# Kernel optimization log

Measured on AMD Instinct MI355X. Metric: run time of the kernel, lower is better.

## Reference

```python
import jax, jax.numpy as jnp
import numpy as np

N_NODES = 50000
N_EDGES = 800000
IN_CH = 128
HIDDEN = [128, 128]
OUT_CH = 64


def _glorot(key, shape):
    fan_in, fan_out = shape
    lim = (6.0 / (fan_in + fan_out)) ** 0.5
    return jax.random.uniform(key, shape, jnp.float32, -lim, lim)


def setup_inputs() -> dict:
    key = jax.random.key(0)
    ks = jax.random.split(key, 12)
    x = jax.random.normal(ks[0], (N_NODES, IN_CH), jnp.float32)
    edge_index = jax.random.randint(ks[1], (2, N_EDGES), 0, N_NODES, jnp.int64)
    dims = [IN_CH] + HIDDEN + [OUT_CH]
    params = {}
    for i in range(len(dims) - 1):
        d_in, d_out = dims[i], dims[i + 1]
        params[f"W_l{i}"] = _glorot(ks[2 + 3 * i], (d_in, d_out))      # neighbor weight
        params[f"W_r{i}"] = _glorot(ks[3 + 3 * i], (d_in, d_out))      # root/self weight
        params[f"b{i}"] = jnp.zeros((d_out,), jnp.float32)
    return {"x": x, "edge_index": edge_index, **params}


def _sage_conv(x, src, dst, W_l, W_r, b):
    # mean-aggregate neighbor features: messages flow src -> dst
    n = x.shape[0]
    agg = jax.ops.segment_sum(x[src], dst, num_segments=n)            # [N, d_in]
    cnt = jax.ops.segment_sum(jnp.ones((src.shape[0],), x.dtype), dst, num_segments=n)
    mean = agg / jnp.maximum(cnt, 1.0)[:, None]
    # PyG SAGEConv: lin_l(mean_neighbors) + lin_r(x_self); bias on lin_l only
    return mean @ W_l + x @ W_r + b


def reference(x, edge_index,
              W_l0, W_r0, b0,
              W_l1, W_r1, b1,
              W_l2, W_r2, b2):
    src, dst = edge_index[0], edge_index[1]
    h = _sage_conv(x, src, dst, W_l0, W_r0, b0)
    h = jax.nn.elu(h)
    h = _sage_conv(h, src, dst, W_l1, W_r1, b1)
    h = jax.nn.elu(h)
    out = _sage_conv(h, src, dst, W_l2, W_r2, b2)
    return out
```

## Files before the change

### kernel.cpp

```cpp
#include <hip/hip_runtime.h>
#include <math.h>

#define N_NODES 50000
#define N_EDGES 800000
#define IN_CH 128
#define NBUCK 196
#define BCAP 5120
#define EPB 4082

typedef unsigned short ushort_t;
typedef unsigned int uint_t;
typedef __attribute__((ext_vector_type(8))) short bf16x8;
typedef __attribute__((ext_vector_type(4))) float f32x4;

static __device__ __forceinline__ ushort_t f32_to_bf16(float f) {
    uint_t u = __float_as_uint(f);
    uint_t r = (u + 0x7fffu + ((u >> 16) & 1u)) >> 16;
    return (ushort_t)r;
}
static __device__ __forceinline__ float bf16_to_f32(ushort_t u) {
    return __uint_as_float(((uint_t)u) << 16);
}

static __device__ __forceinline__ bf16x8 cvt8(const float* __restrict__ p) {
    float4 lo = *(const float4*)p;
    float4 hi = *(const float4*)(p + 4);
    bf16x8 r;
    r[0] = (short)f32_to_bf16(lo.x); r[1] = (short)f32_to_bf16(lo.y);
    r[2] = (short)f32_to_bf16(lo.z); r[3] = (short)f32_to_bf16(lo.w);
    r[4] = (short)f32_to_bf16(hi.x); r[5] = (short)f32_to_bf16(hi.y);
    r[6] = (short)f32_to_bf16(hi.z); r[7] = (short)f32_to_bf16(hi.w);
    return r;
}

__global__ __launch_bounds__(256) void binA(
    const int* __restrict__ src, const int* __restrict__ dst,
    uint_t* __restrict__ gbcnt, uint_t* __restrict__ gbuck) {
    __shared__ uint_t hist[NBUCK];
    __shared__ uint_t excl_s[NBUCK];
    __shared__ uint_t gbase[NBUCK];
    __shared__ uint_t cur[NBUCK];
    __shared__ uint_t pfx[256];
    __shared__ uint_t stage[4096];
    __shared__ uint_t gpos[4096];
    const int t = threadIdx.x;
    const int e0 = blockIdx.x * EPB;
    const int e1 = min(e0 + EPB, N_EDGES);

    for (int i = t; i < NBUCK; i += 256) hist[i] = 0;
    __syncthreads();
    for (int e = e0 + t; e < e1; e += 256) atomicAdd(&hist[dst[e] >> 8], 1u);
    __syncthreads();
    uint_t own = (t < NBUCK) ? hist[t] : 0;
    pfx[t] = own;
    __syncthreads();
    for (int d = 1; d < 256; d <<= 1) {
        uint_t v = (t >= d) ? pfx[t - d] : 0;
        __syncthreads();
        pfx[t] += v;
        __syncthreads();
    }
    if (t < NBUCK) {
        uint_t excl = pfx[t] - own;
        excl_s[t] = excl;
        cur[t] = excl;
        gbase[t] = atomicAdd(&gbcnt[t], own);
    }
    __syncthreads();
    for (int e = e0 + t; e < e1; e += 256) {
        int d_ = dst[e];
        int b = d_ >> 8;
        uint_t p = atomicAdd(&cur[b], 1u);
        stage[p] = ((uint_t)(d_ & 255) << 16) | (uint_t)src[e];
        gpos[p] = (uint_t)b * BCAP + gbase[b] + (p - excl_s[b]);
    }
    __syncthreads();
    const int n = e1 - e0;
    for (int i = t; i < n; i += 256) gbuck[gpos[i]] = stage[i];
}

__global__ __launch_bounds__(256) void binB1(
    const uint_t* __restrict__ gbcnt, const uint_t* __restrict__ gbuck,
    int* __restrict__ degi) {
    __shared__ uint_t h[256];
    const int b = blockIdx.x;
    const int t = threadIdx.x;
    h[t] = 0;
    __syncthreads();
    const uint_t n = gbcnt[b];
    const uint_t* p = &gbuck[(size_t)b * BCAP];
    for (uint_t i = t; i < n; i += 256) atomicAdd(&h[(p[i] >> 16) & 255u], 1u);
    __syncthreads();
    int node = b * 256 + t;
    if (node < N_NODES) degi[node] = (int)h[t];
}

__global__ __launch_bounds__(256) void scan_p1(const int* __restrict__ degi,
                                               int* __restrict__ bsum, int n) {
    __shared__ int s[256];
    const int t = threadIdx.x;
    const int i = blockIdx.x * 256 + t;
    s[t] = (i < n) ? degi[i] : 0;
    __syncthreads();
    for (int d = 128; d > 0; d >>= 1) {
        if (t < d) s[t] += s[t + d];
        __syncthreads();
    }
    if (t == 0) bsum[blockIdx.x] = s[0];
}

__global__ __launch_bounds__(256) void scan_p2(int* __restrict__ bsum, int nb) {
    __shared__ int s[256];
    const int t = threadIdx.x;
    int v = (t < nb) ? bsum[t] : 0;
    s[t] = v;
    __syncthreads();
    for (int d = 1; d < 256; d <<= 1) {
        int u = (t >= d) ? s[t - d] : 0;
        __syncthreads();
        s[t] += u;
        __syncthreads();
    }
    if (t < nb) bsum[t] = s[t] - v;
}

__global__ __launch_bounds__(256) void scan_p3(const int* __restrict__ degi,
                                               const int* __restrict__ bsum,
                                               int* __restrict__ offs, int n) {
    __shared__ int s[256];
    const int t = threadIdx.x;
    const int i = blockIdx.x * 256 + t;
    int v = (i < n) ? degi[i] : 0;
    s[t] = v;
    __syncthreads();
    for (int d = 1; d < 256; d <<= 1) {
        int u = (t >= d) ? s[t - d] : 0;
        __syncthreads();
        s[t] += u;
        __syncthreads();
    }
    if (i < n) offs[i] = s[t] - v + bsum[blockIdx.x];
    if (i == 0) offs[n] = N_EDGES;
}

__global__ __launch_bounds__(256) void binB2(
    const uint_t* __restrict__ gbcnt, const uint_t* __restrict__ gbuck,
    const int* __restrict__ offs, int* __restrict__ ebuf) {
    __shared__ int cur[256];
    __shared__ int stage[BCAP];
    const int b = blockIdx.x;
    const int t = threadIdx.x;
    const int node = b * 256 + t;
    const int obase = offs[b * 256];
    cur[t] = (node < N_NODES) ? (offs[node] - obase) : 0;
    __syncthreads();
    const uint_t n = gbcnt[b];
    const uint_t* p = &gbuck[(size_t)b * BCAP];
    for (uint_t i = t; i < n; i += 256) {
        uint_t pr_ = p[i];
        int l = (pr_ >> 16) & 255;
        int pos = atomicAdd(&cur[l], 1);
        stage[pos] = (int)(pr_ & 0xFFFFu);
    }
    __syncthreads();
    for (uint_t i = t; i < n; i += 256) ebuf[obase + (int)i] = stage[i];
}

template <int D_OUT>
__global__ __launch_bounds__(256) void prep_w(const float* __restrict__ Wl,
                                              const float* __restrict__ Wr,
                                              ushort_t* __restrict__ Bt) {
    int i = blockIdx.x * 256 + threadIdx.x;
    if (i >= 2 * D_OUT * IN_CH) return;
    int c = i / IN_CH, k = i % IN_CH;
    float v = (c < D_OUT) ? Wl[(size_t)k * D_OUT + c] : Wr[(size_t)k * D_OUT + (c - D_OUT)];
    Bt[i] = f32_to_bf16(v);
}

template <int D_OUT, bool IN_F32, bool PL_F32>
__global__ __launch_bounds__(256) void gemm_mfma(
    const void* __restrict__ in_v, const ushort_t* __restrict__ Bt,
    const float* __restrict__ bias,
    void* __restrict__ pl_v, float* __restrict__ pr, int nNodes) {
    constexpr int C = 2 * D_OUT;
    constexpr int SLAB = C / 4;
    constexpr int NI = SLAB / 16;
    const int tid = threadIdx.x;
    const int wave = tid >> 6, lane = tid & 63;
    const int node0 = blockIdx.x * 64;
    const int wcol0 = wave * SLAB;
    const int lrow = lane & 15;
    const int lgrp = lane >> 4;

    const ushort_t* inb = (const ushort_t*)in_v;
    const float* inf = (const float*)in_v;

    f32x4 acc[4][NI] = {};

    for (int ks = 0; ks < 4; ++ks) {
        const int k0 = ks * 32 + lgrp * 8;
        bf16x8 a[4];
#pragma unroll
        for (int mi = 0; mi < 4; ++mi) {
            int r = node0 + mi * 16 + lrow;
            r = min(r, nNodes - 1);
            if (IN_F32) {
                a[mi] = cvt8(&inf[(size_t)r * IN_CH + k0]);
            } else {
                a[mi] = *(const bf16x8*)&inb[(size_t)r * IN_CH + k0];
            }
        }
        bf16x8 bf[NI];
#pragma unroll
        for (int ni = 0; ni < NI; ++ni) {
            int c = wcol0 + ni * 16 + lrow;
            bf[ni] = *(const bf16x8*)&Bt[(size_t)c * IN_CH + k0];
        }
#pragma unroll
        for (int mi = 0; mi < 4; ++mi)
#pragma unroll
            for (int ni = 0; ni < NI; ++ni)
                acc[mi][ni] = __builtin_amdgcn_mfma_f32_16x16x32_bf16(
                    a[mi], bf[ni], acc[mi][ni], 0, 0, 0);
    }

    const bool is_pr = (wcol0 >= D_OUT);
#pragma unroll
    for (int ni = 0; ni < NI; ++ni) {
        const int c = wcol0 + ni * 16 + lrow;
        const float bv = is_pr ? bias[c - D_OUT] : 0.f;
#pragma unroll
        for (int mi = 0; mi < 4; ++mi) {
#pragma unroll
            for (int j = 0; j < 4; ++j) {
                int r = node0 + mi * 16 + lgrp * 4 + j;
                if (r >= nNodes) continue;
                float v = acc[mi][ni][j];
                if (is_pr) {
                    pr[(size_t)r * D_OUT + (c - D_OUT)] = v + bv;
                } else if (PL_F32) {
                    ((float*)pl_v)[(size_t)r * D_OUT + c] = v;
                } else {
                    ((ushort_t*)pl_v)[(size_t)r * D_OUT + c] = f32_to_bf16(v);
                }
            }
        }
    }
}

__global__ __launch_bounds__(256) void gather128_bf16_kernel(
    const int* __restrict__ offs, const int* __restrict__ ebuf,
    const ushort_t* __restrict__ pl, const float* __restrict__ pr,
    ushort_t* __restrict__ out, int nNodes) {
    const int wid = (int)((blockIdx.x * 256u + threadIdx.x) >> 6);
    const int lane = threadIdx.x & 63;
    if (wid >= nNodes) return;
    const int o0 = offs[wid], o1 = offs[wid + 1];
    const float inv = 1.0f / fmaxf((float)(o1 - o0), 1.0f);
    const int c = lane * 2;

    float ax0 = 0, ay0 = 0, ax1 = 0, ay1 = 0, ax2 = 0, ay2 = 0, ax3 = 0, ay3 = 0;
    int j = o0;
    for (; j + 4 <= o1; j += 4) {
        int s0 = ebuf[j], s1 = ebuf[j + 1], s2 = ebuf[j + 2], s3 = ebuf[j + 3];
        uint_t v0 = *(const uint_t*)&pl[(size_t)s0 * 128 + c];
        uint_t v1 = *(const uint_t*)&pl[(size_t)s1 * 128 + c];
        uint_t v2 = *(const uint_t*)&pl[(size_t)s2 * 128 + c];
        uint_t v3 = *(const uint_t*)&pl[(size_t)s3 * 128 + c];
        ax0 += __uint_as_float(v0 << 16); ay0 += __uint_as_float(v0 & 0xffff0000u);
        ax1 += __uint_as_float(v1 << 16); ay1 += __uint_as_float(v1 & 0xffff0000u);
        ax2 += __uint_as_float(v2 << 16); ay2 += __uint_as_float(v2 & 0xffff0000u);
        ax3 += __uint_as_float(v3 << 16); ay3 += __uint_as_float(v3 & 0xffff0000u);
    }
    for (; j < o1; ++j) {
        uint_t v0 = *(const uint_t*)&pl[(size_t)ebuf[j] * 128 + c];
        ax0 += __uint_as_float(v0 << 16);
        ay0 += __uint_as_float(v0 & 0xffff0000u);
    }
    float vx = (ax0 + ax1 + ax2 + ax3) * inv + pr[(size_t)wid * 128 + c];
    float vy = (ay0 + ay1 + ay2 + ay3) * inv + pr[(size_t)wid * 128 + c + 1];
    vx = vx > 0.f ? vx : expm1f(vx);
    vy = vy > 0.f ? vy : expm1f(vy);
    uint_t packed = (uint_t)f32_to_bf16(vx) | ((uint_t)f32_to_bf16(vy) << 16);
    *(uint_t*)&out[(size_t)wid * 128 + c] = packed;
}

__global__ __launch_bounds__(256) void gather64_bf16_kernel(
    const int* __restrict__ offs, const int* __restrict__ ebuf,
    const ushort_t* __restrict__ pl, const float* __restrict__ pr,
    float* __restrict__ out, int nNodes) {
    const int wid = (int)((blockIdx.x * 256u + threadIdx.x) >> 6);
    const int lane = threadIdx.x & 63;
    if (wid >= nNodes) return;
    const int o0 = offs[wid], o1 = offs[wid + 1];
    const float inv = 1.0f / fmaxf((float)(o1 - o0), 1.0f);
    const int c = lane;
    float a0 = 0, a1 = 0, a2 = 0, a3 = 0;
    int j = o0;
    for (; j + 4 <= o1; j += 4) {
        int s0 = ebuf[j], s1 = ebuf[j + 1], s2 = ebuf[j + 2], s3 = ebuf[j + 3];
        a0 += bf16_to_f32(pl[(size_t)s0 * 64 + c]);
        a1 += bf16_to_f32(pl[(size_t)s1 * 64 + c]);
        a2 += bf16_to_f32(pl[(size_t)s2 * 64 + c]);
        a3 += bf16_to_f32(pl[(size_t)s3 * 64 + c]);
    }
    for (; j < o1; ++j) a0 += bf16_to_f32(pl[(size_t)ebuf[j] * 64 + c]);
    float v = (a0 + a1 + a2 + a3) * inv + pr[(size_t)wid * 64 + c];
    out[(size_t)wid * 64 + c] = v;
}

extern "C" void kernel_launch(void* const* d_in, const int* in_sizes, int n_in,
                              void* d_out, int out_size, void* d_ws, size_t ws_size,
                              hipStream_t stream) {
    const float* x = (const float*)d_in[0];
    const int* ei = (const int*)d_in[1];
    const int* src = ei;
    const int* dst = ei + N_EDGES;
    const float* Wl0 = (const float*)d_in[2];
    const float* Wr0 = (const float*)d_in[3];
    const float* b0 = (const float*)d_in[4];
    const float* Wl1 = (const float*)d_in[5];
    const float* Wr1 = (const float*)d_in[6];
    const float* b1 = (const float*)d_in[7];
    const float* Wl2 = (const float*)d_in[8];
    const float* Wr2 = (const float*)d_in[9];
    const float* b2 = (const float*)d_in[10];
    float* out = (float*)d_out;

    int* wsi = (int*)d_ws;
    int* degi = wsi;
    int* offs = degi + 51200;
    int* bsum = offs + 51200;
    uint_t* gbcnt = (uint_t*)(bsum + 256);
    int* ebuf = (int*)(gbcnt + 256);
    uint_t* gbuck = (uint_t*)(ebuf + 800000);
    ushort_t* Bt0 = (ushort_t*)(gbuck + NBUCK * BCAP);
    ushort_t* Bt1 = Bt0 + 256 * 128;
    ushort_t* Bt2 = Bt1 + 256 * 128;
    float* pl = (float*)(Bt2 + 128 * 128);
    const long long NB = (long long)N_NODES * 128;
    float* pr = pl + NB;
    ushort_t* h = (ushort_t*)(pr + NB);

    const int NSB = (N_NODES + 255) / 256;

    hipMemsetAsync(gbcnt, 0, NBUCK * sizeof(uint_t), stream);
    binA<<<NBUCK, 256, 0, stream>>>(src, dst, gbcnt, gbuck);
    binB1<<<NBUCK, 256, 0, stream>>>(gbcnt, gbuck, degi);
    scan_p1<<<NSB, 256, 0, stream>>>(degi, bsum, N_NODES);
    scan_p2<<<1, 256, 0, stream>>>(bsum, NSB);
    scan_p3<<<NSB, 256, 0, stream>>>(degi, bsum, offs, N_NODES);
    binB2<<<NBUCK, 256, 0, stream>>>(gbcnt, gbuck, offs, ebuf);

    prep_w<128><<<(2 * 128 * IN_CH + 255) / 256, 256, 0, stream>>>(Wl0, Wr0, Bt0);
    prep_w<128><<<(2 * 128 * IN_CH + 255) / 256, 256, 0, stream>>>(Wl1, Wr1, Bt1);
    prep_w<64><<<(2 * 64 * IN_CH + 255) / 256, 256, 0, stream>>>(Wl2, Wr2, Bt2);

    const int GEMM_GRID = (N_NODES + 63) / 64;
    const int GATHER_GRID = (N_NODES * 64 + 255) / 256;

    gemm_mfma<128, true, false><<<GEMM_GRID, 256, 0, stream>>>(
        x, Bt0, b0, pl, pr, N_NODES);
    gather128_bf16_kernel<<<GATHER_GRID, 256, 0, stream>>>(
        offs, ebuf, (const ushort_t*)pl, pr, h, N_NODES);

    gemm_mfma<128, false, false><<<GEMM_GRID, 256, 0, stream>>>(
        h, Bt1, b1, pl, pr, N_NODES);
    gather128_bf16_kernel<<<GATHER_GRID, 256, 0, stream>>>(
        offs, ebuf, (const ushort_t*)pl, pr, h, N_NODES);

    gemm_mfma<64, false, false><<<GEMM_GRID, 256, 0, stream>>>(
        h, Bt2, b2, pl, pr, N_NODES);
    gather64_bf16_kernel<<<GATHER_GRID, 256, 0, stream>>>(
        offs, ebuf, (const ushort_t*)pl, pr, out, N_NODES);
}
```

Before: 251.1 us.

## Reorder SAGE layers to aggregate-then-transform with fused concat GEMM

Each layer now gathers the mean of raw bf16 features first, then runs one GEMM over the concatenation [mean, x] against a stacked [W_l; W_r] matrix, with bias and ELU applied in the GEMM epilogue. The input x is converted to bf16 once up front. This removes the fp32 pr intermediate and its read-back in the gather, at the cost of always gathering 128-wide rows, including the last layer, which previously gathered only 64-wide rows, and of an extra mean buffer round trip. GEMM tiling changes to 64x64 blocks over a 2D grid.

After: 248.3 us. About the same (-1.1%).

```diff
diff --git a/kernel.cpp b/kernel.cpp
--- a/kernel.cpp
+++ b/kernel.cpp
@@ -17,20 +17,6 @@
     uint_t u = __float_as_uint(f);
     uint_t r = (u + 0x7fffu + ((u >> 16) & 1u)) >> 16;
     return (ushort_t)r;
-}
-static __device__ __forceinline__ float bf16_to_f32(ushort_t u) {
-    return __uint_as_float(((uint_t)u) << 16);
-}
-
-static __device__ __forceinline__ bf16x8 cvt8(const float* __restrict__ p) {
-    float4 lo = *(const float4*)p;
-    float4 hi = *(const float4*)(p + 4);
-    bf16x8 r;
-    r[0] = (short)f32_to_bf16(lo.x); r[1] = (short)f32_to_bf16(lo.y);
-    r[2] = (short)f32_to_bf16(lo.z); r[3] = (short)f32_to_bf16(lo.w);
-    r[4] = (short)f32_to_bf16(hi.x); r[5] = (short)f32_to_bf16(hi.y);
-    r[6] = (short)f32_to_bf16(hi.z); r[7] = (short)f32_to_bf16(hi.w);
-    return r;
 }
 
 __global__ __launch_bounds__(256) void binA(
@@ -166,92 +152,35 @@
     for (uint_t i = t; i < n; i += 256) ebuf[obase + (int)i] = stage[i];
 }
 
-template <int D_OUT>
+__global__ __launch_bounds__(256) void cvt_x(const float* __restrict__ x,
+                                             ushort_t* __restrict__ xb, int n8) {
+    int i = blockIdx.x * 256 + threadIdx.x;
+    if (i >= n8) return;
+    const float* p = x + (size_t)i * 8;
+    float4 lo = *(const float4*)p;
+    float4 hi = *(const float4*)(p + 4);
+    bf16x8 r;
+    r[0] = (short)f32_to_bf16(lo.x); r[1] = (short)f32_to_bf16(lo.y);
+    r[2] = (short)f32_to_bf16(lo.z); r[3] = (short)f32_to_bf16(lo.w);
+    r[4] = (short)f32_to_bf16(hi.x); r[5] = (short)f32_to_bf16(hi.y);
+    r[6] = (short)f32_to_bf16(hi.z); r[7] = (short)f32_to_bf16(hi.w);
+    *(bf16x8*)&xb[(size_t)i * 8] = r;
+}
+
+template <int C>
 __global__ __launch_bounds__(256) void prep_w(const float* __restrict__ Wl,
                                               const float* __restrict__ Wr,
                                               ushort_t* __restrict__ Bt) {
     int i = blockIdx.x * 256 + threadIdx.x;
-    if (i >= 2 * D_OUT * IN_CH) return;
-    int c = i / IN_CH, k = i % IN_CH;
-    float v = (c < D_OUT) ? Wl[(size_t)k * D_OUT + c] : Wr[(size_t)k * D_OUT + (c - D_OUT)];
+    if (i >= C * 256) return;
+    int c = i / 256, k = i % 256;
+    float v = (k < 128) ? Wl[(size_t)k * C + c] : Wr[(size_t)(k - 128) * C + c];
     Bt[i] = f32_to_bf16(v);
 }
 
-template <int D_OUT, bool IN_F32, bool PL_F32>
-__global__ __launch_bounds__(256) void gemm_mfma(
-    const void* __restrict__ in_v, const ushort_t* __restrict__ Bt,
-    const float* __restrict__ bias,
-    void* __restrict__ pl_v, float* __restrict__ pr, int nNodes) {
-    constexpr int C = 2 * D_OUT;
-    constexpr int SLAB = C / 4;
-    constexpr int NI = SLAB / 16;
-    const int tid = threadIdx.x;
-    const int wave = tid >> 6, lane = tid & 63;
-    const int node0 = blockIdx.x * 64;
-    const int wcol0 = wave * SLAB;
-    const int lrow = lane & 15;
-    const int lgrp = lane >> 4;
-
-    const ushort_t* inb = (const ushort_t*)in_v;
-    const float* inf = (const float*)in_v;
-
-    f32x4 acc[4][NI] = {};
-
-    for (int ks = 0; ks < 4; ++ks) {
-        const int k0 = ks * 32 + lgrp * 8;
-        bf16x8 a[4];
-#pragma unroll
-        for (int mi = 0; mi < 4; ++mi) {
-            int r = node0 + mi * 16 + lrow;
-            r = min(r, nNodes - 1);
-            if (IN_F32) {
-                a[mi] = cvt8(&inf[(size_t)r * IN_CH + k0]);
-            } else {
-                a[mi] = *(const bf16x8*)&inb[(size_t)r * IN_CH + k0];
-            }
-        }
-        bf16x8 bf[NI];
-#pragma unroll
-        for (int ni = 0; ni < NI; ++ni) {
-            int c = wcol0 + ni * 16 + lrow;
-            bf[ni] = *(const bf16x8*)&Bt[(size_t)c * IN_CH + k0];
-        }
-#pragma unroll
-        for (int mi = 0; mi < 4; ++mi)
-#pragma unroll
-            for (int ni = 0; ni < NI; ++ni)
-                acc[mi][ni] = __builtin_amdgcn_mfma_f32_16x16x32_bf16(
-                    a[mi], bf[ni], acc[mi][ni], 0, 0, 0);
-    }
-
-    const bool is_pr = (wcol0 >= D_OUT);
-#pragma unroll
-    for (int ni = 0; ni < NI; ++ni) {
-        const int c = wcol0 + ni * 16 + lrow;
-        const float bv = is_pr ? bias[c - D_OUT] : 0.f;
-#pragma unroll
-        for (int mi = 0; mi < 4; ++mi) {
-#pragma unroll
-            for (int j = 0; j < 4; ++j) {
-                int r = node0 + mi * 16 + lgrp * 4 + j;
-                if (r >= nNodes) continue;
-                float v = acc[mi][ni][j];
-                if (is_pr) {
-                    pr[(size_t)r * D_OUT + (c - D_OUT)] = v + bv;
-                } else if (PL_F32) {
-                    ((float*)pl_v)[(size_t)r * D_OUT + c] = v;
-                } else {
-                    ((ushort_t*)pl_v)[(size_t)r * D_OUT + c] = f32_to_bf16(v);
-                }
-            }
-        }
-    }
-}
-
-__global__ __launch_bounds__(256) void gather128_bf16_kernel(
+__global__ __launch_bounds__(256) void gather_mean(
     const int* __restrict__ offs, const int* __restrict__ ebuf,
-    const ushort_t* __restrict__ pl, const float* __restrict__ pr,
-    ushort_t* __restrict__ out, int nNodes) {
+    const ushort_t* __restrict__ feat, ushort_t* __restrict__ M, int nNodes) {
     const int wid = (int)((blockIdx.x * 256u + threadIdx.x) >> 6);
     const int lane = threadIdx.x & 63;
     if (wid >= nNodes) return;
@@ -263,50 +192,83 @@
     int j = o0;
     for (; j + 4 <= o1; j += 4) {
         int s0 = ebuf[j], s1 = ebuf[j + 1], s2 = ebuf[j + 2], s3 = ebuf[j + 3];
-        uint_t v0 = *(const uint_t*)&pl[(size_t)s0 * 128 + c];
-        uint_t v1 = *(const uint_t*)&pl[(size_t)s1 * 128 + c];
-        uint_t v2 = *(const uint_t*)&pl[(size_t)s2 * 128 + c];
-        uint_t v3 = *(const uint_t*)&pl[(size_t)s3 * 128 + c];
+        uint_t v0 = *(const uint_t*)&feat[(size_t)s0 * 128 + c];
+        uint_t v1 = *(const uint_t*)&feat[(size_t)s1 * 128 + c];
+        uint_t v2 = *(const uint_t*)&feat[(size_t)s2 * 128 + c];
+        uint_t v3 = *(const uint_t*)&feat[(size_t)s3 * 128 + c];
         ax0 += __uint_as_float(v0 << 16); ay0 += __uint_as_float(v0 & 0xffff0000u);
         ax1 += __uint_as_float(v1 << 16); ay1 += __uint_as_float(v1 & 0xffff0000u);
         ax2 += __uint_as_float(v2 << 16); ay2 += __uint_as_float(v2 & 0xffff0000u);
         ax3 += __uint_as_float(v3 << 16); ay3 += __uint_as_float(v3 & 0xffff0000u);
     }
     for (; j < o1; ++j) {
-        uint_t v0 = *(const uint_t*)&pl[(size_t)ebuf[j] * 128 + c];
+        uint_t v0 = *(const uint_t*)&feat[(size_t)ebuf[j] * 128 + c];
         ax0 += __uint_as_float(v0 << 16);
         ay0 += __uint_as_float(v0 & 0xffff0000u);
     }
-    float vx = (ax0 + ax1 + ax2 + ax3) * inv + pr[(size_t)wid * 128 + c];
-    float vy = (ay0 + ay1 + ay2 + ay3) * inv + pr[(size_t)wid * 128 + c + 1];
-    vx = vx > 0.f ? vx : expm1f(vx);
-    vy = vy > 0.f ? vy : expm1f(vy);
+    float vx = (ax0 + ax1 + ax2 + ax3) * inv;
+    float vy = (ay0 + ay1 + ay2 + ay3) * inv;
     uint_t packed = (uint_t)f32_to_bf16(vx) | ((uint_t)f32_to_bf16(vy) << 16);
-    *(uint_t*)&out[(size_t)wid * 128 + c] = packed;
-}
-
-__global__ __launch_bounds__(256) void gather64_bf16_kernel(
-    const int* __restrict__ offs, const int* __restrict__ ebuf,
-    const ushort_t* __restrict__ pl, const float* __restrict__ pr,
-    float* __restrict__ out, int nNodes) {
-    const int wid = (int)((blockIdx.x * 256u + threadIdx.x) >> 6);
-    const int lane = threadIdx.x & 63;
-    if (wid >= nNodes) return;
-    const int o0 = offs[wid], o1 = offs[wid + 1];
-    const float inv = 1.0f / fmaxf((float)(o1 - o0), 1.0f);
-    const int c = lane;
-    float a0 = 0, a1 = 0, a2 = 0, a3 = 0;
-    int j = o0;
-    for (; j + 4 <= o1; j += 4) {
-        int s0 = ebuf[j], s1 = ebuf[j + 1], s2 = ebuf[j + 2], s3 = ebuf[j + 3];
-        a0 += bf16_to_f32(pl[(size_t)s0 * 64 + c]);
-        a1 += bf16_to_f32(pl[(size_t)s1 * 64 + c]);
-        a2 += bf16_to_f32(pl[(size_t)s2 * 64 + c]);
-        a3 += bf16_to_f32(pl[(size_t)s3 * 64 + c]);
-    }
-    for (; j < o1; ++j) a0 += bf16_to_f32(pl[(size_t)ebuf[j] * 64 + c]);
-    float v = (a0 + a1 + a2 + a3) * inv + pr[(size_t)wid * 64 + c];
-    out[(size_t)wid * 64 + c] = v;
+    *(uint_t*)&M[(size_t)wid * 128 + c] = packed;
+}
+
+template <int C, bool ELU, bool OUT_F32>
+__global__ __launch_bounds__(256) void gemm_fused(
+    const ushort_t* __restrict__ M, const ushort_t* __restrict__ X,
+    const ushort_t* __restrict__ Bt, const float* __restrict__ bias,
+    void* __restrict__ out_v, int nNodes) {
+    const int tid = threadIdx.x;
+    const int wave = tid >> 6, lane = tid & 63;
+    const int lrow = lane & 15, lgrp = lane >> 4;
+    const int rowbase = blockIdx.x * 64 + (wave >> 1) * 32;
+    const int colbase = blockIdx.y * 64 + (wave & 1) * 32;
+
+    f32x4 acc[2][2] = {};
+
+#pragma unroll
+    for (int half = 0; half < 2; ++half) {
+        const ushort_t* A = half ? X : M;
+#pragma unroll
+        for (int ks = 0; ks < 4; ++ks) {
+            const int k0 = ks * 32 + lgrp * 8;
+            bf16x8 a[2], bf[2];
+#pragma unroll
+            for (int mi = 0; mi < 2; ++mi) {
+                int r = rowbase + mi * 16 + lrow;
+                r = min(r, nNodes - 1);
+                a[mi] = *(const bf16x8*)&A[(size_t)r * 128 + k0];
+            }
+#pragma unroll
+            for (int ni = 0; ni < 2; ++ni) {
+                int c = colbase + ni * 16 + lrow;
+                bf[ni] = *(const bf16x8*)&Bt[(size_t)c * 256 + half * 128 + k0];
+            }
+#pragma unroll
+            for (int mi = 0; mi < 2; ++mi)
+#pragma unroll
+                for (int ni = 0; ni < 2; ++ni)
+                    acc[mi][ni] = __builtin_amdgcn_mfma_f32_16x16x32_bf16(
+                        a[mi], bf[ni], acc[mi][ni], 0, 0, 0);
+        }
+    }
+
+#pragma unroll
+    for (int ni = 0; ni < 2; ++ni) {
+        const int c = colbase + ni * 16 + lrow;
+        const float bv = bias[c];
+#pragma unroll
+        for (int mi = 0; mi < 2; ++mi) {
+#pragma unroll
+            for (int j = 0; j < 4; ++j) {
+                int r = rowbase + mi * 16 + lgrp * 4 + j;
+                if (r >= nNodes) continue;
+                float v = acc[mi][ni][j] + bv;
+                if (ELU) v = v > 0.f ? v : expm1f(v);
+                if (OUT_F32) ((float*)out_v)[(size_t)r * C + c] = v;
+                else ((ushort_t*)out_v)[(size_t)r * C + c] = f32_to_bf16(v);
+            }
+        }
+    }
 }
 
 extern "C" void kernel_launch(void* const* d_in, const int* in_sizes, int n_in,
@@ -335,12 +297,13 @@
     int* ebuf = (int*)(gbcnt + 256);
     uint_t* gbuck = (uint_t*)(ebuf + 800000);
     ushort_t* Bt0 = (ushort_t*)(gbuck + NBUCK * BCAP);
-    ushort_t* Bt1 = Bt0 + 256 * 128;
-    ushort_t* Bt2 = Bt1 + 256 * 128;
-    float* pl = (float*)(Bt2 + 128 * 128);
+    ushort_t* Bt1 = Bt0 + 128 * 256;
+    ushort_t* Bt2 = Bt1 + 128 * 256;
     const long long NB = (long long)N_NODES * 128;
-    float* pr = pl + NB;
-    ushort_t* h = (ushort_t*)(pr + NB);
+    ushort_t* xb = Bt2 + 64 * 256;
+    ushort_t* Mb = xb + NB;
+    ushort_t* hA = Mb + NB;
+    ushort_t* hB = hA + NB;
 
     const int NSB = (N_NODES + 255) / 256;
 
@@ -352,25 +315,23 @@
     scan_p3<<<NSB, 256, 0, stream>>>(degi, bsum, offs, N_NODES);
     binB2<<<NBUCK, 256, 0, stream>>>(gbcnt, gbuck, offs, ebuf);
 
-    prep_w<128><<<(2 * 128 * IN_CH + 255) / 256, 256, 0, stream>>>(Wl0, Wr0, Bt0);
-    prep_w<128><<<(2 * 128 * IN_CH + 255) / 256, 256, 0, stream>>>(Wl1, Wr1, Bt1);
-    prep_w<64><<<(2 * 64 * IN_CH + 255) / 256, 256, 0, stream>>>(Wl2, Wr2, Bt2);
-
-    const int GEMM_GRID = (N_NODES + 63) / 64;
+    cvt_x<<<(N_NODES * 16 + 255) / 256, 256, 0, stream>>>(x, xb, N_NODES * 16);
+    prep_w<128><<<(128 * 256 + 255) / 256, 256, 0, stream>>>(Wl0, Wr0, Bt0);
+    prep_w<128><<<(128 * 256 + 255) / 256, 256, 0, stream>>>(Wl1, Wr1, Bt1);
+    prep_w<64><<<(64 * 256 + 255) / 256, 256, 0, stream>>>(Wl2, Wr2, Bt2);
+
     const int GATHER_GRID = (N_NODES * 64 + 255) / 256;
-
-    gemm_mfma<128, true, false><<<GEMM_GRID, 256, 0, stream>>>(
-        x, Bt0, b0, pl, pr, N_NODES);
-    gather128_bf16_kernel<<<GATHER_GRID, 256, 0, stream>>>(
-        offs, ebuf, (const ushort_t*)pl, pr, h, N_NODES);
-
-    gemm_mfma<128, false, false><<<GEMM_GRID, 256, 0, stream>>>(
-        h, Bt1, b1, pl, pr, N_NODES);
-    gather128_bf16_kernel<<<GATHER_GRID, 256, 0, stream>>>(
-        offs, ebuf, (const ushort_t*)pl, pr, h, N_NODES);
-
-    gemm_mfma<64, false, false><<<GEMM_GRID, 256, 0, stream>>>(
-        h, Bt2, b2, pl, pr, N_NODES);
-    gather64_bf16_kernel<<<GATHER_GRID, 256, 0, stream>>>(
-        offs, ebuf, (const ushort_t*)pl, pr, out, N_NODES);
-}
+    const int GR = (N_NODES + 63) / 64;
+
+    gather_mean<<<GATHER_GRID, 256, 0, stream>>>(offs, ebuf, xb, Mb, N_NODES);
+    gemm_fused<128, true, false><<<dim3(GR, 2), 256, 0, stream>>>(
+        Mb, xb, Bt0, b0, hA, N_NODES);
+
+    gather_mean<<<GATHER_GRID, 256, 0, stream>>>(offs, ebuf, hA, Mb, N_NODES);
+    gemm_fused<128, true, false><<<dim3(GR, 2), 256, 0, stream>>>(
+        Mb, hA, Bt1, b1, hB, N_NODES);
+
+    gather_mean<<<GATHER_GRID, 256, 0, stream>>>(offs, ebuf, hB, Mb, N_NODES);
+    gemm_fused<64, false, true><<<dim3(GR, 1), 256, 0, stream>>>(
+        Mb, hB, Bt2, b2, out, N_NODES);
+}
```
